# Kernel tuning notes

Measured on AMD Instinct MI355X. Metric: run time of the kernel, lower is better.

The kernel has to match this reference:

```python
import jax, jax.numpy as jnp
import numpy as np

TEMPERATURE = 0.03


def setup_inputs() -> dict:
    key = jax.random.key(0)
    k1, k2, k3 = jax.random.split(key, 3)
    B, d = 8192, 256
    z_a = jax.random.normal(k1, (B, d), dtype=jnp.float32)
    z_t = jax.random.normal(k2, (B, d), dtype=jnp.float32)
    # module expects L2-normalized projections
    z_a = z_a / jnp.linalg.norm(z_a, axis=-1, keepdims=True)
    z_t = z_t / jnp.linalg.norm(z_t, axis=-1, keepdims=True)
    patient_ids = jax.random.randint(k3, (B,), 0, 2048, dtype=jnp.int64)
    return {"z_a": z_a, "z_t": z_t, "patient_ids": patient_ids}


def _direction_loss(sim, cross_mask):
    # sim: (B, B) row i = anchor i vs all candidates; cross_mask: (B, B) valid negatives
    B = sim.shape[0]
    pos = jnp.diagonal(sim)                              # (B,) positive logits
    logit_mask = cross_mask | jnp.eye(B, dtype=bool)     # negatives + the positive
    lse = jax.nn.logsumexp(sim, axis=1, where=logit_mask)  # (B,)
    row_loss = lse - pos                                 # CE with label = positive
    valid = cross_mask.any(axis=1)                       # rows with >=1 cross-patient neg
    cnt = jnp.sum(valid)
    total = jnp.sum(jnp.where(valid, row_loss, 0.0))
    return jnp.where(cnt > 0, total / jnp.maximum(cnt, 1).astype(sim.dtype), 0.0)


def reference(z_a, z_t, patient_ids):
    sim = jnp.matmul(z_a, z_t.T) / TEMPERATURE           # (B, B)
    cross = patient_ids[:, None] != patient_ids[None, :] # cross-patient negative mask
    loss_a2t = _direction_loss(sim, cross)
    loss_t2a = _direction_loss(sim.T, cross.T)
    return (loss_a2t + loss_t2a) / 2.0
```

## Files before the change

kernel.cpp:

```cpp
#include <hip/hip_runtime.h>
#include <math.h>

#define BSZ    8192
#define DDIM   256
#define SCALE  33.33333333333333f
#define C_OFF  34.0f
#define SC_L2E 48.08983470f
#define C2     49.05163139f

typedef float floatx4 __attribute__((ext_vector_type(4)));
typedef long long fp8x8;

__device__ __forceinline__ fp8x8 cvt8_f8(const float* __restrict__ g)
{
    const float4 lo = *(const float4*)g;
    const float4 hi = *(const float4*)(g + 4);
    int a = __builtin_amdgcn_cvt_pk_fp8_f32(lo.x, lo.y, 0, false);
    a     = __builtin_amdgcn_cvt_pk_fp8_f32(lo.z, lo.w, a, true);
    int b = __builtin_amdgcn_cvt_pk_fp8_f32(hi.x, hi.y, 0, false);
    b     = __builtin_amdgcn_cvt_pk_fp8_f32(hi.z, hi.w, b, true);
    int2 r; r.x = a; r.y = b;
    return *(fp8x8*)&r;
}

__global__ __launch_bounds__(256) void prep_kernel(
    const float* __restrict__ za, const float* __restrict__ zt,
    unsigned char* __restrict__ za_f8, unsigned char* __restrict__ zt_perm,
    float* __restrict__ zbase)
{
    const int bid = blockIdx.x, tid = threadIdx.x;
    if (bid < 1024) {
        const int i = (bid * 256 + tid) * 8;
        *(fp8x8*)(za_f8 + i) = cvt8_f8(za + i);
        if (bid < 16) {
            const int z = bid * 1024 + tid * 4;
            *(float4*)&zbase[z] = (float4){0.f, 0.f, 0.f, 0.f};
            if (bid == 0 && tid == 0) {
                zbase[16384] = 0.f;
                ((int*)zbase)[16385] = 0;
                ((int*)zbase)[16386] = 0;
            }
        }
    } else {
        const int S     = (bid - 1024) * 256 + tid;
        const int chunk = S >> 9, P = S & 511;
        const int col   = P >> 2, sp = P & 3;
        const int sl    = sp ^ ((col >> 2) & 3);
        const int cb    = chunk >> 3, kc = chunk & 7;
        const float* src = zt + (size_t)(cb * 128 + col) * DDIM + kc * 32 + sl * 8;
        *(fp8x8*)(zt_perm + (size_t)S * 8) = cvt8_f8(src);
    }
}

__global__ __launch_bounds__(256, 2) void sim_fused(
    const unsigned char* __restrict__ za_f8, const unsigned char* __restrict__ zt_perm,
    const int* __restrict__ pid,
    float* __restrict__ s_row, float* __restrict__ s_col,
    float* __restrict__ posv)
{
    __shared__ __align__(16) unsigned char Bs[3][16384];
    __shared__ int   pidc[512];
    __shared__ float colsum[512];

    const int bid   = blockIdx.x;
    const int strip = bid & 15, band = bid >> 4;
    const int row0  = band * 128, scol0 = strip * 512;
    const int tid   = threadIdx.x, lane = tid & 63, wid = tid >> 6;
    const int q     = lane >> 4, lc = lane & 15;
    const int rbase = row0 + wid * 32;
    const int qs8   = (q ^ ((lc >> 2) & 3)) * 8;

    pidc[tid]         = pid[scol0 + tid];
    pidc[tid + 256]   = pid[scol0 + tid + 256];
    colsum[tid]       = 0.f;
    colsum[tid + 256] = 0.f;

    fp8x8 af[2][8];
    #pragma unroll
    for (int m = 0; m < 2; m++) {
        const unsigned char* ga = za_f8 + (size_t)(rbase + m * 16 + lc) * DDIM + q * 8;
        #pragma unroll
        for (int kc = 0; kc < 8; kc++)
            af[m][kc] = *(const fp8x8*)(ga + kc * 32);
    }

    int prw[2][4];
    #pragma unroll
    for (int m = 0; m < 2; m++)
        #pragma unroll
        for (int r = 0; r < 4; r++)
            prw[m][r] = pid[rbase + m * 16 + q * 4 + r];

    const unsigned char* zp = zt_perm + (size_t)(strip * 32) * 4096
                            + wid * 4096 + lane * 16;

#define STAGE(C, bufi)                                                           \
    do {                                                                         \
        const unsigned char* _s = zp + (size_t)(C) * 16384;                      \
        unsigned char* _d = &Bs[0][0] + (bufi) * 16384 + wid * 4096;             \
        _Pragma("unroll")                                                        \
        for (int _i = 0; _i < 4; _i++)                                           \
            __builtin_amdgcn_global_load_lds(                                    \
                (const __attribute__((address_space(1))) void*)(_s + _i * 1024), \
                (__attribute__((address_space(3))) void*)(_d + _i * 1024),       \
                16, 0, 0);                                                       \
    } while (0)

    STAGE(0, 0);
    __syncthreads();

    float rowp[8] = {0.f, 0.f, 0.f, 0.f, 0.f, 0.f, 0.f, 0.f};
    const int diag_t = (row0 - scol0) >> 7;
    int bcur = 0;

    for (int t = 0; t < 4; t++) {
        floatx4 acc[2][8];
        #pragma unroll
        for (int m = 0; m < 2; m++)
            #pragma unroll
            for (int n = 0; n < 8; n++)
                acc[m][n] = (floatx4){0.f, 0.f, 0.f, 0.f};

        #pragma unroll
        for (int c2 = 0; c2 < 2; c2++) {
            const int C    = t * 2 + c2;
            const int bnxt = (bcur == 2) ? 0 : bcur + 1;
            if (C < 7) {
                STAGE(C + 1, bnxt);
                __asm__ volatile("s_waitcnt vmcnt(4)" ::: "memory");
            } else {
                __asm__ volatile("s_waitcnt vmcnt(0)" ::: "memory");
            }
            __asm__ volatile("s_barrier" ::: "memory");

            const unsigned char* B = &Bs[0][0] + bcur * 16384;
            #pragma unroll
            for (int j = 0; j < 4; j++) {
                const int kc = c2 * 4 + j;
                fp8x8 bfr[8];
                #pragma unroll
                for (int n = 0; n < 8; n++)
                    bfr[n] = *(const fp8x8*)(B + j * 4096 + (n * 16 + lc) * 32 + qs8);

                #pragma unroll
                for (int m = 0; m < 2; m++)
                    #pragma unroll
                    for (int n = 0; n < 8; n++)
                        acc[m][n] = __builtin_amdgcn_mfma_f32_16x16x32_fp8_fp8(
                            af[m][kc], bfr[n], acc[m][n], 0, 0, 0);
            }
            bcur = bnxt;
        }

        int pc[8];
        #pragma unroll
        for (int n = 0; n < 8; n++) pc[n] = pidc[t * 128 + n * 16 + lc];

        float colp[8] = {0.f, 0.f, 0.f, 0.f, 0.f, 0.f, 0.f, 0.f};
        #pragma unroll
        for (int m = 0; m < 2; m++) {
            #pragma unroll
            for (int r = 0; r < 4; r++) {
                const int pr = prw[m][r];
                float rsum = 0.f;
                #pragma unroll
                for (int n = 0; n < 8; n++) {
                    float e = __builtin_amdgcn_exp2f(fmaf(acc[m][n][r], SC_L2E, -C2));
                    e = (pr != pc[n]) ? e : 0.f;
                    rsum += e;
                    colp[n] += e;
                }
                rowp[m * 4 + r] += rsum;
            }
        }

        if (t == diag_t) {
            #pragma unroll
            for (int m = 0; m < 2; m++) {
                const int nstar = wid * 2 + m;
                #pragma unroll
                for (int r = 0; r < 4; r++) {
                    float v = 0.f;
                    #pragma unroll
                    for (int n = 0; n < 8; n++)
                        v = (n == nstar) ? acc[m][n][r] : v;
                    float e = __builtin_amdgcn_exp2f(fmaf(v, SC_L2E, -C2));
                    const bool own = (lc == q * 4 + r);
                    e = own ? e : 0.f;
                    rowp[m * 4 + r] += e;
                    #pragma unroll
                    for (int n = 0; n < 8; n++)
                        colp[n] += (n == nstar) ? e : 0.f;
                    if (own) posv[rbase + m * 16 + q * 4 + r] = v * SCALE;
                }
            }
        }

        #pragma unroll
        for (int n = 0; n < 8; n++) {
            colp[n] += __shfl_xor(colp[n], 16, 64);
            colp[n] += __shfl_xor(colp[n], 32, 64);
        }
        if (q == 0) {
            #pragma unroll
            for (int n = 0; n < 8; n++)
                atomicAdd(&colsum[t * 128 + n * 16 + lc], colp[n]);
        }
    }

    #pragma unroll
    for (int i = 0; i < 8; i++) {
        rowp[i] += __shfl_xor(rowp[i], 1, 64);
        rowp[i] += __shfl_xor(rowp[i], 2, 64);
        rowp[i] += __shfl_xor(rowp[i], 4, 64);
        rowp[i] += __shfl_xor(rowp[i], 8, 64);
    }
    float rw = rowp[0];
    #pragma unroll
    for (int idx = 1; idx < 8; idx++)
        rw = (lc == idx) ? rowp[idx] : rw;
    if (lc < 8)
        atomicAdd(&s_row[rbase + (lc >> 2) * 16 + q * 4 + (lc & 3)], rw);

    __syncthreads();
    atomicAdd(&s_col[scol0 + tid], colsum[tid]);
    atomicAdd(&s_col[scol0 + tid + 256], colsum[tid + 256]);
#undef STAGE
}

__global__ __launch_bounds__(256) void finalize_rows(
    const int* __restrict__ pid,
    const float* __restrict__ s_row, const float* __restrict__ s_col,
    const float* __restrict__ posv,
    float* __restrict__ total, int* __restrict__ flag, int* __restrict__ cnt,
    float* __restrict__ out)
{
    const int i = blockIdx.x * 256 + threadIdx.x;
    const float p = posv[i];
    const float c = (logf(s_row[i]) + C_OFF - p)
                  + (logf(s_col[i]) + C_OFF - p);

    float v = c;
    #pragma unroll
    for (int off = 32; off > 0; off >>= 1) v += __shfl_down(v, off, 64);
    if ((threadIdx.x & 63) == 0) atomicAdd(total, v);

    const unsigned long long m = __ballot(pid[i] != pid[0]);
    if (m != 0ull && (threadIdx.x & 63) == 0) atomicOr(flag, 1);

    __syncthreads();
    __threadfence();
    if (threadIdx.x == 0) {
        const int done = atomicAdd(cnt, 1);
        if (done == (int)gridDim.x - 1) {
            const float t = atomicAdd(total, 0.0f);
            const int   f = atomicOr(flag, 0);
            out[0] = f ? t / (2.0f * (float)BSZ) : 0.0f;
        }
    }
}

extern "C" void kernel_launch(void* const* d_in, const int* in_sizes, int n_in,
                              void* d_out, int out_size, void* d_ws, size_t ws_size,
                              hipStream_t stream)
{
    const float* za  = (const float*)d_in[0];
    const float* zt  = (const float*)d_in[1];
    const int*   pid = (const int*)d_in[2];
    float* out = (float*)d_out;

    unsigned char* za_f8   = (unsigned char*)d_ws;
    unsigned char* zt_perm = za_f8 + (size_t)BSZ * DDIM;
    float*  s_row   = (float*)(zt_perm + (size_t)BSZ * DDIM);
    float*  s_col   = s_row + BSZ;
    float*  total   = s_col + BSZ;
    int*    flag    = (int*)(total + 1);
    int*    cnt     = flag + 1;
    float*  posv    = (float*)(cnt + 1);

    prep_kernel<<<dim3(2048), 256, 0, stream>>>(za, zt, za_f8, zt_perm, s_row);

    sim_fused<<<dim3(1024), 256, 0, stream>>>(za_f8, zt_perm, pid,
                                              s_row, s_col, posv);

    finalize_rows<<<dim3(BSZ / 256), 256, 0, stream>>>(
        pid, s_row, s_col, posv, total, flag, cnt, out);
}
```

Baseline: 118.7 us.

## Load B fragments directly from global memory instead of LDS triple buffering

Drops the 48KB LDS triple-buffer staging of the permuted fp8 z_t tiles. Each wave now reads its MFMA B fragments straight from global memory (through the caches), which removes the per-chunk barriers and waitcnt synchronisation. Launch bounds go from 2 to 4 blocks per CU to use the freed LDS for occupancy. The cost is four waves redundantly fetching the same B data from L1/L2 with no software prefetch, and the tighter register budget may cause spills.

```diff
diff --git a/kernel.cpp b/kernel.cpp
--- a/kernel.cpp
+++ b/kernel.cpp
@@ -52,13 +52,12 @@
     }
 }
 
-__global__ __launch_bounds__(256, 2) void sim_fused(
+__global__ __launch_bounds__(256, 4) void sim_fused(
     const unsigned char* __restrict__ za_f8, const unsigned char* __restrict__ zt_perm,
     const int* __restrict__ pid,
     float* __restrict__ s_row, float* __restrict__ s_col,
     float* __restrict__ posv)
 {
-    __shared__ __align__(16) unsigned char Bs[3][16384];
     __shared__ int   pidc[512];
     __shared__ float colsum[512];
 
@@ -91,27 +90,12 @@
         for (int r = 0; r < 4; r++)
             prw[m][r] = pid[rbase + m * 16 + q * 4 + r];
 
-    const unsigned char* zp = zt_perm + (size_t)(strip * 32) * 4096
-                            + wid * 4096 + lane * 16;
-
-#define STAGE(C, bufi)                                                           \
-    do {                                                                         \
-        const unsigned char* _s = zp + (size_t)(C) * 16384;                      \
-        unsigned char* _d = &Bs[0][0] + (bufi) * 16384 + wid * 4096;             \
-        _Pragma("unroll")                                                        \
-        for (int _i = 0; _i < 4; _i++)                                           \
-            __builtin_amdgcn_global_load_lds(                                    \
-                (const __attribute__((address_space(1))) void*)(_s + _i * 1024), \
-                (__attribute__((address_space(3))) void*)(_d + _i * 1024),       \
-                16, 0, 0);                                                       \
-    } while (0)
-
-    STAGE(0, 0);
     __syncthreads();
+
+    const unsigned char* bb = zt_perm + (size_t)strip * 131072 + lc * 32 + qs8;
 
     float rowp[8] = {0.f, 0.f, 0.f, 0.f, 0.f, 0.f, 0.f, 0.f};
     const int diag_t = (row0 - scol0) >> 7;
-    int bcur = 0;
 
     for (int t = 0; t < 4; t++) {
         floatx4 acc[2][8];
@@ -123,24 +107,14 @@
 
         #pragma unroll
         for (int c2 = 0; c2 < 2; c2++) {
-            const int C    = t * 2 + c2;
-            const int bnxt = (bcur == 2) ? 0 : bcur + 1;
-            if (C < 7) {
-                STAGE(C + 1, bnxt);
-                __asm__ volatile("s_waitcnt vmcnt(4)" ::: "memory");
-            } else {
-                __asm__ volatile("s_waitcnt vmcnt(0)" ::: "memory");
-            }
-            __asm__ volatile("s_barrier" ::: "memory");
-
-            const unsigned char* B = &Bs[0][0] + bcur * 16384;
+            const unsigned char* bc = bb + (size_t)(t * 2 + c2) * 16384;
             #pragma unroll
             for (int j = 0; j < 4; j++) {
                 const int kc = c2 * 4 + j;
                 fp8x8 bfr[8];
                 #pragma unroll
                 for (int n = 0; n < 8; n++)
-                    bfr[n] = *(const fp8x8*)(B + j * 4096 + (n * 16 + lc) * 32 + qs8);
+                    bfr[n] = *(const fp8x8*)(bc + j * 4096 + n * 512);
 
                 #pragma unroll
                 for (int m = 0; m < 2; m++)
@@ -149,7 +123,6 @@
                         acc[m][n] = __builtin_amdgcn_mfma_f32_16x16x32_fp8_fp8(
                             af[m][kc], bfr[n], acc[m][n], 0, 0, 0);
             }
-            bcur = bnxt;
         }
 
         int pc[8];
@@ -225,7 +198,6 @@
     __syncthreads();
     atomicAdd(&s_col[scol0 + tid], colsum[tid]);
     atomicAdd(&s_col[scol0 + tid + 256], colsum[tid + 256]);
-#undef STAGE
 }
 
 __global__ __launch_bounds__(256) void finalize_rows(
```

Result: slower. 145.0 us (+22.2%).
